# Kernel optimization log

Measured on AMD Instinct MI355X. Metric: run time of the kernel, lower is better.

The kernel has to match this reference:

```python
import jax, jax.numpy as jnp
import numpy as np

N, E = 50000, 800000
C, NT, ET, H, D = 128, 8, 16, 64, 4
TOTAL_IN = 2 * C + 2 * NT + ET  # 288
EPS = 1e-5


def setup_inputs() -> dict:
    key = jax.random.key(0)
    ks = jax.random.split(key, 10)
    x = jax.random.normal(ks[0], (N, C), dtype=jnp.float32)
    edge_index = jax.random.randint(ks[1], (2, E), 0, N, dtype=jnp.int64)
    edge_types = jax.random.randint(ks[2], (E,), 0, ET, dtype=jnp.int64)
    node_types = jax.random.randint(ks[3], (N,), 0, NT, dtype=jnp.int64)
    ln_w = jnp.ones((TOTAL_IN,), dtype=jnp.float32)
    ln_b = jnp.zeros((TOTAL_IN,), dtype=jnp.float32)
    W1 = jax.random.normal(ks[4], (TOTAL_IN, H), dtype=jnp.float32) * 0.05
    b1 = jnp.zeros((H,), dtype=jnp.float32)
    W2 = jax.random.normal(ks[5], (H, D * D), dtype=jnp.float32) * 0.05
    b2 = jnp.zeros((D * D,), dtype=jnp.float32)
    return {"x": x, "edge_index": edge_index, "edge_types": edge_types,
            "node_types": node_types, "ln_w": ln_w, "ln_b": ln_b,
            "W1": W1, "b1": b1, "W2": W2, "b2": b2}


def reference(x, edge_index, edge_types, node_types, ln_w, ln_b, W1, b1, W2, b2):
    row, col = edge_index[0], edge_index[1]
    # edge gathers of node features and one-hot type encodings
    nt_oh = jax.nn.one_hot(node_types, NT, dtype=x.dtype)   # [N, NT]
    et_oh = jax.nn.one_hot(edge_types, ET, dtype=x.dtype)   # [E, ET]
    h = jnp.concatenate([x[row], x[col], nt_oh[row], nt_oh[col], et_oh], axis=-1)  # [E, 288]
    # LayerNorm
    mu = jnp.mean(h, axis=-1, keepdims=True)
    var = jnp.mean(jnp.square(h - mu), axis=-1, keepdims=True)
    h = (h - mu) * jax.lax.rsqrt(var + EPS) * ln_w + ln_b
    # small MLP
    h = jax.nn.relu(h @ W1 + b1) @ W2 + b2          # [E, D*D]
    h = h.reshape(-1, D, D)
    att = jax.nn.softmax(h, axis=-1)                 # row-stochastic per edge
    return jnp.eye(D, dtype=h.dtype)[None] - att     # [E, D, D]
```

## Files before the change

### kernel.cpp

```cpp
#include <hip/hip_runtime.h>
#include <hip/hip_bf16.h>

#define NN 50000
#define NE 800000
#define C 128
#define HH 64
#define TIN 288
#define LN_EPS 1e-5f

typedef __attribute__((ext_vector_type(8))) short bf16x8;
typedef __attribute__((ext_vector_type(4))) float f32x4;

#define ETT_OFF 512
#define B1F_OFF 2560
#define B2F_OFF 35328
#define OHU_OFF 37376
#define OHV_OFF 38400
#define SQ_OFF 39424
#define U_OFF 439424
#define V_OFF 6839424

__device__ __forceinline__ short f2bf(float f) {
    __hip_bfloat16 h = __float2bfloat16(f);
    return __builtin_bit_cast(short, h);
}
__device__ __forceinline__ float bf2f(short s) {
    unsigned int u = ((unsigned int)(unsigned short)s) << 16;
    return __builtin_bit_cast(float, u);
}

__global__ void prep_weights(const float* __restrict__ ln_w,
                             const float* __restrict__ ln_b,
                             const float* __restrict__ W1,
                             const float* __restrict__ b1,
                             const float* __restrict__ W2,
                             float* __restrict__ ws) {
    int gid = blockIdx.x * 256 + threadIdx.x;
    if (blockIdx.x == 0 && threadIdx.x < 64) {
        int l = threadIdx.x;
        float s = 0.f, c = 0.f;
        for (int k = 0; k < TIN; ++k) {
            float w = W1[k * HH + l];
            s += ln_w[k] * w;
            c += ln_b[k] * w;
        }
        ws[l] = s;
        ws[64 + l] = c + b1[l];
    }
    short* B1 = (short*)((char*)ws + B1F_OFF);
    for (int idx = gid; idx < 16384; idx += 8192) {
        int j = idx & 7, l = (idx >> 3) & 63, cc = (idx >> 9) & 3, kt = idx >> 11;
        int g = l >> 4, m = l & 15;
        int k = 32 * kt + 8 * g + j, n = 16 * cc + m;
        B1[idx] = f2bf(ln_w[k] * W1[k * HH + n]);
    }
    short* B2 = (short*)((char*)ws + B2F_OFF);
    for (int idx = gid; idx < 1024; idx += 8192) {
        int j = idx & 7, l = (idx >> 3) & 63, kt = idx >> 9;
        int g = l >> 4, m = l & 15;
        int k = 32 * kt + 8 * g + j;
        B2[idx] = f2bf(W2[k * 16 + m]);
    }
    short* ohu = (short*)((char*)ws + OHU_OFF);
    short* ohv = (short*)((char*)ws + OHV_OFF);
    for (int idx = gid; idx < 512; idx += 8192) {
        int t = idx >> 6, j = idx & 63;
        ohu[idx] = f2bf(ln_w[256 + t] * W1[(256 + t) * HH + j]);
        ohv[idx] = f2bf(ln_w[264 + t] * W1[(264 + t) * HH + j]);
    }
    short* ett = (short*)((char*)ws + ETT_OFF);
    for (int idx = gid; idx < 1024; idx += 8192) {
        int et = idx >> 6, j = idx & 63;
        int unit = (j >> 3) ^ (et & 7);
        ett[et * 64 + unit * 8 + (j & 7)] = f2bf(ln_w[272 + et] * W1[(272 + et) * HH + j]);
    }
}

__global__ __launch_bounds__(512) void node_uv(const float* __restrict__ x,
                                               const int* __restrict__ ntype,
                                               float* __restrict__ ws) {
    __shared__ __align__(16) short lds_n[16384 + 8 * 1024];
    int tid = threadIdx.x;
    {
        const float4* src = (const float4*)((const char*)ws + B1F_OFF);
        float4* dst = (float4*)lds_n;
        for (int i = tid; i < 2048; i += 512) dst[i] = src[i];
    }
    __syncthreads();

    int wave = tid >> 6, lane = tid & 63, m = lane & 15, g = lane >> 4;
    int tile = blockIdx.x * 128 + wave * 16;
    int n = tile + m;
    int nc = n < NN ? n : NN - 1;

    float sum = 0.f, sq = 0.f;
    bf16x8 a[4];
#pragma unroll
    for (int kt = 0; kt < 4; ++kt) {
        const float* p = x + (size_t)nc * C + kt * 32 + g * 8;
        float4 p0 = *(const float4*)p;
        float4 p1 = *(const float4*)(p + 4);
        float vv[8] = {p0.x, p0.y, p0.z, p0.w, p1.x, p1.y, p1.z, p1.w};
#pragma unroll
        for (int j = 0; j < 8; ++j) {
            sum += vv[j];
            sq = fmaf(vv[j], vv[j], sq);
            a[kt][j] = f2bf(vv[j]);
        }
    }
    sum += __shfl_xor(sum, 16); sum += __shfl_xor(sum, 32);
    sq  += __shfl_xor(sq, 16);  sq  += __shfl_xor(sq, 32);
    if (g == 0 && n < NN)
        ((float2*)((char*)ws + SQ_OFF))[n] = make_float2(sum, sq);

    f32x4 au[4], av[4];
#pragma unroll
    for (int cc = 0; cc < 4; ++cc) { au[cc] = (f32x4){0,0,0,0}; av[cc] = (f32x4){0,0,0,0}; }
#pragma unroll
    for (int kt = 0; kt < 4; ++kt) {
        const bf16x8* Bu = (const bf16x8*)(lds_n + (kt * 4) * 512);
        const bf16x8* Bv = (const bf16x8*)(lds_n + ((kt + 4) * 4) * 512);
#pragma unroll
        for (int cc = 0; cc < 4; ++cc) {
            au[cc] = __builtin_amdgcn_mfma_f32_16x16x32_bf16(a[kt], Bu[cc * 64 + lane], au[cc], 0, 0, 0);
            av[cc] = __builtin_amdgcn_mfma_f32_16x16x32_bf16(a[kt], Bv[cc * 64 + lane], av[cc], 0, 0, 0);
        }
    }

    int ntv[4];
#pragma unroll
    for (int i = 0; i < 4; ++i) {
        int nn = tile + 4 * g + i;
        ntv[i] = ntype[nn < NN ? nn : NN - 1];
    }
    const unsigned short* ohu = (const unsigned short*)((const char*)ws + OHU_OFF);
    const unsigned short* ohv = (const unsigned short*)((const char*)ws + OHV_OFF);
    unsigned short* uT = (unsigned short*)((char*)ws + U_OFF);
    unsigned short* vT = (unsigned short*)((char*)ws + V_OFF);
    short* tb = lds_n + 16384 + wave * 1024;
    int nst = tile + m;

#pragma unroll
    for (int cc = 0; cc < 4; ++cc)
#pragma unroll
        for (int i = 0; i < 4; ++i) {
            float val = au[cc][i] + bf2f((short)ohu[ntv[i] * 64 + 16 * cc + m]);
            int r16 = 4 * g + i;
            tb[(r16 * 64 + 16 * cc + m) ^ ((r16 & 7) << 3)] = f2bf(val);
        }
    if (nst < NN) {
#pragma unroll
        for (int s2 = 0; s2 < 2; ++s2) {
            int idx = (m * 64 + 16 * g + 8 * s2) ^ ((m & 7) << 3);
            *(bf16x8*)(uT + (size_t)nst * 64 + 16 * g + 8 * s2) = *(const bf16x8*)(tb + idx);
        }
    }
#pragma unroll
    for (int cc = 0; cc < 4; ++cc)
#pragma unroll
        for (int i = 0; i < 4; ++i) {
            float val = av[cc][i] + bf2f((short)ohv[ntv[i] * 64 + 16 * cc + m]);
            int r16 = 4 * g + i;
            tb[(r16 * 64 + 16 * cc + m) ^ ((r16 & 7) << 3)] = f2bf(val);
        }
    if (nst < NN) {
#pragma unroll
        for (int s2 = 0; s2 < 2; ++s2) {
            int idx = (m * 64 + 16 * g + 8 * s2) ^ ((m & 7) << 3);
            *(bf16x8*)(vT + (size_t)nst * 64 + 16 * g + 8 * s2) = *(const bf16x8*)(tb + idx);
        }
    }
}

__global__ __launch_bounds__(512, 3) void edge_kernel(
    const int* __restrict__ ei,
    const int* __restrict__ etype,
    const float* __restrict__ ws,
    const float* __restrict__ b2,
    float* __restrict__ out) {
    __shared__ __align__(16) short lds_e[2048];
    int tid = threadIdx.x;
    int wave = tid >> 6, lane = tid & 63, m = lane & 15, g = lane >> 4;
    int base = blockIdx.x * 256 + wave * 32;
    int e0 = base + m, e1 = base + 16 + m;

    int row0 = ei[e0], col0 = ei[NE + e0], et0 = etype[e0];
    int row1 = ei[e1], col1 = ei[NE + e1], et1 = etype[e1];

    if (tid < 128)
        ((float4*)lds_e)[tid] = *(const float4*)((const char*)ws + B2F_OFF + tid * 16);
    else if (tid < 256)
        ((float4*)lds_e)[tid] = *(const float4*)((const char*)ws + ETT_OFF + (tid - 128) * 16);
    __syncthreads();

    const float2* SQ = (const float2*)((const char*)ws + SQ_OFF);
    float2 sqr0 = SQ[row0], sqc0 = SQ[col0];
    float2 sqr1 = SQ[row1], sqc1 = SQ[col1];
    const unsigned short* uT = (const unsigned short*)((const char*)ws + U_OFF);
    const unsigned short* vT = (const unsigned short*)((const char*)ws + V_OFF);
    bf16x8 U00 = *(const bf16x8*)(uT + (size_t)row0 * 64 + 8 * g);
    bf16x8 U01 = *(const bf16x8*)(uT + (size_t)row0 * 64 + 32 + 8 * g);
    bf16x8 V00 = *(const bf16x8*)(vT + (size_t)col0 * 64 + 8 * g);
    bf16x8 V01 = *(const bf16x8*)(vT + (size_t)col0 * 64 + 32 + 8 * g);
    bf16x8 U10 = *(const bf16x8*)(uT + (size_t)row1 * 64 + 8 * g);
    bf16x8 U11 = *(const bf16x8*)(uT + (size_t)row1 * 64 + 32 + 8 * g);
    bf16x8 V10 = *(const bf16x8*)(vT + (size_t)col1 * 64 + 8 * g);
    bf16x8 V11 = *(const bf16x8*)(vT + (size_t)col1 * 64 + 32 + 8 * g);
    f32x4 s00 = *(const f32x4*)(ws + 8 * g);
    f32x4 s01 = *(const f32x4*)(ws + 8 * g + 4);
    f32x4 s10 = *(const f32x4*)(ws + 32 + 8 * g);
    f32x4 s11 = *(const f32x4*)(ws + 36 + 8 * g);
    f32x4 c00 = *(const f32x4*)(ws + 64 + 8 * g);
    f32x4 c01 = *(const f32x4*)(ws + 64 + 8 * g + 4);
    f32x4 c10 = *(const f32x4*)(ws + 96 + 8 * g);
    f32x4 c11 = *(const f32x4*)(ws + 100 + 8 * g);
    float4 b2q = *(const float4*)(b2 + 4 * g);
    asm volatile("" ::: "memory");

    const bf16x8* W2A = (const bf16x8*)lds_e;
    bf16x8 w0 = W2A[lane], w1 = W2A[64 + lane];
    const short* ett = lds_e + 1024;

#pragma unroll
    for (int t = 0; t < 2; ++t) {
        int et = t ? et1 : et0;
        float2 sqr = t ? sqr1 : sqr0, sqc = t ? sqc1 : sqc0;
        bf16x8 U0 = t ? U10 : U00, U1 = t ? U11 : U01;
        bf16x8 V0 = t ? V10 : V00, V1 = t ? V11 : V01;

        bf16x8 T0 = *(const bf16x8*)(ett + et * 64 + ((g ^ (et & 7)) << 3));
        bf16x8 T1 = *(const bf16x8*)(ett + et * 64 + (((4 + g) ^ (et & 7)) << 3));

        float mu = (sqr.x + sqc.x + 3.0f) * (1.0f / TIN);
        float var = (sqr.y + sqc.y + 3.0f) * (1.0f / TIN) - mu * mu;
        float rstd = rsqrtf(var + LN_EPS);
        float rm = rstd * mu;

        bf16x8 af0, af1;
#pragma unroll
        for (int j = 0; j < 4; ++j) {
            float tt = bf2f(U0[j]) + bf2f(V0[j]) + bf2f(T0[j]);
            float h = fmaf(rstd, tt, fmaf(-rm, s00[j], c00[j]));
            af0[j] = f2bf(fmaxf(h, 0.f));
            float tt2 = bf2f(U0[j + 4]) + bf2f(V0[j + 4]) + bf2f(T0[j + 4]);
            float h2 = fmaf(rstd, tt2, fmaf(-rm, s01[j], c01[j]));
            af0[j + 4] = f2bf(fmaxf(h2, 0.f));
            float tt3 = bf2f(U1[j]) + bf2f(V1[j]) + bf2f(T1[j]);
            float h3 = fmaf(rstd, tt3, fmaf(-rm, s10[j], c10[j]));
            af1[j] = f2bf(fmaxf(h3, 0.f));
            float tt4 = bf2f(U1[j + 4]) + bf2f(V1[j + 4]) + bf2f(T1[j + 4]);
            float h4 = fmaf(rstd, tt4, fmaf(-rm, s11[j], c11[j]));
            af1[j + 4] = f2bf(fmaxf(h4, 0.f));
        }

        f32x4 o = {0.f, 0.f, 0.f, 0.f};
        o = __builtin_amdgcn_mfma_f32_16x16x32_bf16(w0, af0, o, 0, 0, 0);
        o = __builtin_amdgcn_mfma_f32_16x16x32_bf16(w1, af1, o, 0, 0, 0);

        float v0 = o[0] + b2q.x, v1 = o[1] + b2q.y;
        float v2 = o[2] + b2q.z, v3 = o[3] + b2q.w;
        float mx = fmaxf(fmaxf(v0, v1), fmaxf(v2, v3));
        float x0 = __expf(v0 - mx), x1 = __expf(v1 - mx);
        float x2 = __expf(v2 - mx), x3 = __expf(v3 - mx);
        float inv = 1.0f / (x0 + x1 + x2 + x3);
        float4 res;
        res.x = (g == 0 ? 1.0f : 0.0f) - x0 * inv;
        res.y = (g == 1 ? 1.0f : 0.0f) - x1 * inv;
        res.z = (g == 2 ? 1.0f : 0.0f) - x2 * inv;
        res.w = (g == 3 ? 1.0f : 0.0f) - x3 * inv;
        *(float4*)(out + (size_t)(base + 16 * t + m) * 16 + 4 * g) = res;
    }
}

extern "C" void kernel_launch(void* const* d_in, const int* in_sizes, int n_in,
                              void* d_out, int out_size, void* d_ws, size_t ws_size,
                              hipStream_t stream) {
    const float* x     = (const float*)d_in[0];
    const int*   ei    = (const int*)d_in[1];
    const int*   etype = (const int*)d_in[2];
    const int*   ntype = (const int*)d_in[3];
    const float* ln_w  = (const float*)d_in[4];
    const float* ln_b  = (const float*)d_in[5];
    const float* W1    = (const float*)d_in[6];
    const float* b1    = (const float*)d_in[7];
    const float* W2    = (const float*)d_in[8];
    const float* b2    = (const float*)d_in[9];
    float* out = (float*)d_out;
    float* ws  = (float*)d_ws;

    prep_weights<<<32, 256, 0, stream>>>(ln_w, ln_b, W1, b1, W2, ws);
    node_uv<<<(NN + 127) / 128, 512, 0, stream>>>(x, ntype, ws);
    edge_kernel<<<NE / 256, 512, 0, stream>>>(ei, etype, ws, b2, out);
}
```

Baseline: 78.52 us.

## Store per-node U/V projections as fp8 to halve edge gather traffic

The per-node first-layer projections U and V are quantized to fp8 (e4m3) instead of bf16. The node kernel uses a new LDS transpose layout matched to how the edge kernel unpacks them, and the edge kernel decodes them with packed fp8-to-f32 conversions. This halves the bytes of the random row/col gathers that dominate the edge kernel. It also adds nontemporal loads and stores for streaming data and drops the occupancy hint on the edge kernel. In exchange it loses precision in the hidden activations, which may affect accuracy tolerance.

```diff
diff --git a/kernel.cpp b/kernel.cpp
--- a/kernel.cpp
+++ b/kernel.cpp
@@ -10,6 +10,8 @@
 
 typedef __attribute__((ext_vector_type(8))) short bf16x8;
 typedef __attribute__((ext_vector_type(4))) float f32x4;
+typedef __attribute__((ext_vector_type(2))) float f32x2;
+typedef __attribute__((ext_vector_type(4))) int i32x4;
 
 #define ETT_OFF 512
 #define B1F_OFF 2560
@@ -18,7 +20,7 @@
 #define OHV_OFF 38400
 #define SQ_OFF 39424
 #define U_OFF 439424
-#define V_OFF 6839424
+#define V_OFF 3639424
 
 __device__ __forceinline__ short f2bf(float f) {
     __hip_bfloat16 h = __float2bfloat16(f);
@@ -79,11 +81,11 @@
 __global__ __launch_bounds__(512) void node_uv(const float* __restrict__ x,
                                                const int* __restrict__ ntype,
                                                float* __restrict__ ws) {
-    __shared__ __align__(16) short lds_n[16384 + 8 * 1024];
+    __shared__ __align__(16) char lds_n[32768 + 8192];
     int tid = threadIdx.x;
     {
-        const float4* src = (const float4*)((const char*)ws + B1F_OFF);
-        float4* dst = (float4*)lds_n;
+        const f32x4* src = (const f32x4*)((const char*)ws + B1F_OFF);
+        f32x4* dst = (f32x4*)lds_n;
         for (int i = tid; i < 2048; i += 512) dst[i] = src[i];
     }
     __syncthreads();
@@ -98,9 +100,9 @@
 #pragma unroll
     for (int kt = 0; kt < 4; ++kt) {
         const float* p = x + (size_t)nc * C + kt * 32 + g * 8;
-        float4 p0 = *(const float4*)p;
-        float4 p1 = *(const float4*)(p + 4);
-        float vv[8] = {p0.x, p0.y, p0.z, p0.w, p1.x, p1.y, p1.z, p1.w};
+        f32x4 p0 = __builtin_nontemporal_load((const f32x4*)p);
+        f32x4 p1 = __builtin_nontemporal_load((const f32x4*)(p + 4));
+        float vv[8] = {p0[0], p0[1], p0[2], p0[3], p1[0], p1[1], p1[2], p1[3]};
 #pragma unroll
         for (int j = 0; j < 8; ++j) {
             sum += vv[j];
@@ -118,8 +120,8 @@
     for (int cc = 0; cc < 4; ++cc) { au[cc] = (f32x4){0,0,0,0}; av[cc] = (f32x4){0,0,0,0}; }
 #pragma unroll
     for (int kt = 0; kt < 4; ++kt) {
-        const bf16x8* Bu = (const bf16x8*)(lds_n + (kt * 4) * 512);
-        const bf16x8* Bv = (const bf16x8*)(lds_n + ((kt + 4) * 4) * 512);
+        const bf16x8* Bu = (const bf16x8*)(lds_n + (kt * 4) * 1024);
+        const bf16x8* Bv = (const bf16x8*)(lds_n + ((kt + 4) * 4) * 1024);
 #pragma unroll
         for (int cc = 0; cc < 4; ++cc) {
             au[cc] = __builtin_amdgcn_mfma_f32_16x16x32_bf16(a[kt], Bu[cc * 64 + lane], au[cc], 0, 0, 0);
@@ -135,44 +137,53 @@
     }
     const unsigned short* ohu = (const unsigned short*)((const char*)ws + OHU_OFF);
     const unsigned short* ohv = (const unsigned short*)((const char*)ws + OHV_OFF);
-    unsigned short* uT = (unsigned short*)((char*)ws + U_OFF);
-    unsigned short* vT = (unsigned short*)((char*)ws + V_OFF);
-    short* tb = lds_n + 16384 + wave * 1024;
+    char* u8 = (char*)ws + U_OFF;
+    char* v8 = (char*)ws + V_OFF;
+    char* tb8 = lds_n + 32768 + wave * 1024;
     int nst = tile + m;
+    int k2 = m >> 2;
 
 #pragma unroll
     for (int cc = 0; cc < 4; ++cc)
 #pragma unroll
         for (int i = 0; i < 4; ++i) {
             float val = au[cc][i] + bf2f((short)ohu[ntv[i] * 64 + 16 * cc + m]);
-            int r16 = 4 * g + i;
-            tb[(r16 * 64 + 16 * cc + m) ^ ((r16 & 7) << 3)] = f2bf(val);
+            int d = 16 * cc + m;
+            int pos = (d < 32) ? (16 * (d >> 3) + (d & 7))
+                               : (16 * ((d - 32) >> 3) + 8 + ((d - 32) & 7));
+            pos ^= (g << 4);
+            int pk = __builtin_amdgcn_cvt_pk_fp8_f32(val, val, 0, false);
+            tb8[(4 * g + i) * 64 + pos] = (char)(pk & 0xFF);
         }
     if (nst < NN) {
-#pragma unroll
-        for (int s2 = 0; s2 < 2; ++s2) {
-            int idx = (m * 64 + 16 * g + 8 * s2) ^ ((m & 7) << 3);
-            *(bf16x8*)(uT + (size_t)nst * 64 + 16 * g + 8 * s2) = *(const bf16x8*)(tb + idx);
-        }
+        i32x4 val = *(const i32x4*)(tb8 + m * 64 + 16 * (g ^ k2));
+        *(i32x4*)(u8 + (size_t)nst * 64 + 16 * g) = val;
     }
 #pragma unroll
     for (int cc = 0; cc < 4; ++cc)
 #pragma unroll
         for (int i = 0; i < 4; ++i) {
             float val = av[cc][i] + bf2f((short)ohv[ntv[i] * 64 + 16 * cc + m]);
-            int r16 = 4 * g + i;
-            tb[(r16 * 64 + 16 * cc + m) ^ ((r16 & 7) << 3)] = f2bf(val);
+            int d = 16 * cc + m;
+            int pos = (d < 32) ? (16 * (d >> 3) + (d & 7))
+                               : (16 * ((d - 32) >> 3) + 8 + ((d - 32) & 7));
+            pos ^= (g << 4);
+            int pk = __builtin_amdgcn_cvt_pk_fp8_f32(val, val, 0, false);
+            tb8[(4 * g + i) * 64 + pos] = (char)(pk & 0xFF);
         }
     if (nst < NN) {
-#pragma unroll
-        for (int s2 = 0; s2 < 2; ++s2) {
-            int idx = (m * 64 + 16 * g + 8 * s2) ^ ((m & 7) << 3);
-            *(bf16x8*)(vT + (size_t)nst * 64 + 16 * g + 8 * s2) = *(const bf16x8*)(tb + idx);
-        }
-    }
-}
-
-__global__ __launch_bounds__(512, 3) void edge_kernel(
+        i32x4 val = *(const i32x4*)(tb8 + m * 64 + 16 * (g ^ k2));
+        *(i32x4*)(v8 + (size_t)nst * 64 + 16 * g) = val;
+    }
+}
+
+__device__ __forceinline__ void dec4(int w, float* o) {
+    f32x2 lo = __builtin_amdgcn_cvt_pk_f32_fp8(w, false);
+    f32x2 hi = __builtin_amdgcn_cvt_pk_f32_fp8(w, true);
+    o[0] = lo[0]; o[1] = lo[1]; o[2] = hi[0]; o[3] = hi[1];
+}
+
+__global__ __launch_bounds__(512) void edge_kernel(
     const int* __restrict__ ei,
     const int* __restrict__ etype,
     const float* __restrict__ ws,
@@ -184,28 +195,28 @@
     int base = blockIdx.x * 256 + wave * 32;
     int e0 = base + m, e1 = base + 16 + m;
 
-    int row0 = ei[e0], col0 = ei[NE + e0], et0 = etype[e0];
-    int row1 = ei[e1], col1 = ei[NE + e1], et1 = etype[e1];
+    int row0 = __builtin_nontemporal_load(ei + e0);
+    int col0 = __builtin_nontemporal_load(ei + NE + e0);
+    int et0  = __builtin_nontemporal_load(etype + e0);
+    int row1 = __builtin_nontemporal_load(ei + e1);
+    int col1 = __builtin_nontemporal_load(ei + NE + e1);
+    int et1  = __builtin_nontemporal_load(etype + e1);
 
     if (tid < 128)
-        ((float4*)lds_e)[tid] = *(const float4*)((const char*)ws + B2F_OFF + tid * 16);
+        ((f32x4*)lds_e)[tid] = *(const f32x4*)((const char*)ws + B2F_OFF + tid * 16);
     else if (tid < 256)
-        ((float4*)lds_e)[tid] = *(const float4*)((const char*)ws + ETT_OFF + (tid - 128) * 16);
+        ((f32x4*)lds_e)[tid] = *(const f32x4*)((const char*)ws + ETT_OFF + (tid - 128) * 16);
     __syncthreads();
 
     const float2* SQ = (const float2*)((const char*)ws + SQ_OFF);
     float2 sqr0 = SQ[row0], sqc0 = SQ[col0];
     float2 sqr1 = SQ[row1], sqc1 = SQ[col1];
-    const unsigned short* uT = (const unsigned short*)((const char*)ws + U_OFF);
-    const unsigned short* vT = (const unsigned short*)((const char*)ws + V_OFF);
-    bf16x8 U00 = *(const bf16x8*)(uT + (size_t)row0 * 64 + 8 * g);
-    bf16x8 U01 = *(const bf16x8*)(uT + (size_t)row0 * 64 + 32 + 8 * g);
-    bf16x8 V00 = *(const bf16x8*)(vT + (size_t)col0 * 64 + 8 * g);
-    bf16x8 V01 = *(const bf16x8*)(vT + (size_t)col0 * 64 + 32 + 8 * g);
-    bf16x8 U10 = *(const bf16x8*)(uT + (size_t)row1 * 64 + 8 * g);
-    bf16x8 U11 = *(const bf16x8*)(uT + (size_t)row1 * 64 + 32 + 8 * g);
-    bf16x8 V10 = *(const bf16x8*)(vT + (size_t)col1 * 64 + 8 * g);
-    bf16x8 V11 = *(const bf16x8*)(vT + (size_t)col1 * 64 + 32 + 8 * g);
+    const char* u8 = (const char*)ws + U_OFF;
+    const char* v8 = (const char*)ws + V_OFF;
+    i32x4 u0q = *(const i32x4*)(u8 + (size_t)row0 * 64 + 16 * g);
+    i32x4 v0q = *(const i32x4*)(v8 + (size_t)col0 * 64 + 16 * g);
+    i32x4 u1q = *(const i32x4*)(u8 + (size_t)row1 * 64 + 16 * g);
+    i32x4 v1q = *(const i32x4*)(v8 + (size_t)col1 * 64 + 16 * g);
     f32x4 s00 = *(const f32x4*)(ws + 8 * g);
     f32x4 s01 = *(const f32x4*)(ws + 8 * g + 4);
     f32x4 s10 = *(const f32x4*)(ws + 32 + 8 * g);
@@ -214,7 +225,7 @@
     f32x4 c01 = *(const f32x4*)(ws + 64 + 8 * g + 4);
     f32x4 c10 = *(const f32x4*)(ws + 96 + 8 * g);
     f32x4 c11 = *(const f32x4*)(ws + 100 + 8 * g);
-    float4 b2q = *(const float4*)(b2 + 4 * g);
+    f32x4 b2q = *(const f32x4*)(b2 + 4 * g);
     asm volatile("" ::: "memory");
 
     const bf16x8* W2A = (const bf16x8*)lds_e;
@@ -225,11 +236,15 @@
     for (int t = 0; t < 2; ++t) {
         int et = t ? et1 : et0;
         float2 sqr = t ? sqr1 : sqr0, sqc = t ? sqc1 : sqc0;
-        bf16x8 U0 = t ? U10 : U00, U1 = t ? U11 : U01;
-        bf16x8 V0 = t ? V10 : V00, V1 = t ? V11 : V01;
+        i32x4 uq = t ? u1q : u0q;
+        i32x4 vq = t ? v1q : v0q;
 
         bf16x8 T0 = *(const bf16x8*)(ett + et * 64 + ((g ^ (et & 7)) << 3));
         bf16x8 T1 = *(const bf16x8*)(ett + et * 64 + (((4 + g) ^ (et & 7)) << 3));
+
+        float uf[16], vf[16];
+        dec4(uq[0], uf); dec4(uq[1], uf + 4); dec4(uq[2], uf + 8); dec4(uq[3], uf + 12);
+        dec4(vq[0], vf); dec4(vq[1], vf + 4); dec4(vq[2], vf + 8); dec4(vq[3], vf + 12);
 
         float mu = (sqr.x + sqc.x + 3.0f) * (1.0f / TIN);
         float var = (sqr.y + sqc.y + 3.0f) * (1.0f / TIN) - mu * mu;
@@ -239,16 +254,16 @@
         bf16x8 af0, af1;
 #pragma unroll
         for (int j = 0; j < 4; ++j) {
-            float tt = bf2f(U0[j]) + bf2f(V0[j]) + bf2f(T0[j]);
+            float tt = uf[j] + vf[j] + bf2f(T0[j]);
             float h = fmaf(rstd, tt, fmaf(-rm, s00[j], c00[j]));
             af0[j] = f2bf(fmaxf(h, 0.f));
-            float tt2 = bf2f(U0[j + 4]) + bf2f(V0[j + 4]) + bf2f(T0[j + 4]);
+            float tt2 = uf[j + 4] + vf[j + 4] + bf2f(T0[j + 4]);
             float h2 = fmaf(rstd, tt2, fmaf(-rm, s01[j], c01[j]));
             af0[j + 4] = f2bf(fmaxf(h2, 0.f));
-            float tt3 = bf2f(U1[j]) + bf2f(V1[j]) + bf2f(T1[j]);
+            float tt3 = uf[j + 8] + vf[j + 8] + bf2f(T1[j]);
             float h3 = fmaf(rstd, tt3, fmaf(-rm, s10[j], c10[j]));
             af1[j] = f2bf(fmaxf(h3, 0.f));
-            float tt4 = bf2f(U1[j + 4]) + bf2f(V1[j + 4]) + bf2f(T1[j + 4]);
+            float tt4 = uf[j + 12] + vf[j + 12] + bf2f(T1[j + 4]);
             float h4 = fmaf(rstd, tt4, fmaf(-rm, s11[j], c11[j]));
             af1[j + 4] = f2bf(fmaxf(h4, 0.f));
         }
@@ -257,18 +272,18 @@
         o = __builtin_amdgcn_mfma_f32_16x16x32_bf16(w0, af0, o, 0, 0, 0);
         o = __builtin_amdgcn_mfma_f32_16x16x32_bf16(w1, af1, o, 0, 0, 0);
 
-        float v0 = o[0] + b2q.x, v1 = o[1] + b2q.y;
-        float v2 = o[2] + b2q.z, v3 = o[3] + b2q.w;
+        float v0 = o[0] + b2q[0], v1 = o[1] + b2q[1];
+        float v2 = o[2] + b2q[2], v3 = o[3] + b2q[3];
         float mx = fmaxf(fmaxf(v0, v1), fmaxf(v2, v3));
         float x0 = __expf(v0 - mx), x1 = __expf(v1 - mx);
         float x2 = __expf(v2 - mx), x3 = __expf(v3 - mx);
         float inv = 1.0f / (x0 + x1 + x2 + x3);
-        float4 res;
-        res.x = (g == 0 ? 1.0f : 0.0f) - x0 * inv;
-        res.y = (g == 1 ? 1.0f : 0.0f) - x1 * inv;
-        res.z = (g == 2 ? 1.0f : 0.0f) - x2 * inv;
-        res.w = (g == 3 ? 1.0f : 0.0f) - x3 * inv;
-        *(float4*)(out + (size_t)(base + 16 * t + m) * 16 + 4 * g) = res;
+        f32x4 res;
+        res[0] = (g == 0 ? 1.0f : 0.0f) - x0 * inv;
+        res[1] = (g == 1 ? 1.0f : 0.0f) - x1 * inv;
+        res[2] = (g == 2 ? 1.0f : 0.0f) - x2 * inv;
+        res[3] = (g == 3 ? 1.0f : 0.0f) - x3 * inv;
+        __builtin_nontemporal_store(res, (f32x4*)(out + (size_t)(base + 16 * t + m) * 16 + 4 * g));
     }
 }
 
```

Result: faster. 69.43 us (-11.6%).
